# Optimization experiments

Hardware: AMD Instinct MI355X
Metric: run time of the kernel (lower is better)

## Reference

```python
import jax, jax.numpy as jnp
import numpy as np

B, S, D, H, HZ = 4096, 64, 9, 128, 32
DT = 0.1


def _lstm_cell(x, h, c, Wih, Whh, bih, bhh):
    gates = x @ Wih.T + bih + h @ Whh.T + bhh
    i, f, g, o = jnp.split(gates, 4, axis=-1)
    c_new = jax.nn.sigmoid(f) * c + jax.nn.sigmoid(i) * jnp.tanh(g)
    h_new = jax.nn.sigmoid(o) * jnp.tanh(c_new)
    return h_new, c_new


def _forward(input_batch, W_ih_enc, W_hh_enc, b_ih_enc, b_hh_enc, W_e, V_e, v_e,
             W_d, V_d, v_d, W_ih_dec, W_hh_dec, b_ih_dec, b_hh_dec,
             W_out, b_out, scaler_mean, scaler_std, pos_mean):
    bsz = input_batch.shape[0]
    # ---- encoder with input attention ----
    x_perm = jnp.swapaxes(input_batch, 1, 2)          # (B, D, S)
    attn_input = jnp.einsum('bds,ts->bdt', x_perm, V_e)  # V_e * x^i, precomputed once
    h0 = jnp.zeros((bsz, H), input_batch.dtype)
    c0 = jnp.zeros((bsz, H), input_batch.dtype)

    def enc_step(carry, x_t):
        h, c = carry
        attn_hidden = jnp.concatenate([h, c], axis=1) @ W_e.T          # (B, S)
        comb = jnp.tanh(attn_hidden[:, None, :] + attn_input)          # (B, D, S)
        e = comb @ v_e                                                 # (B, D)
        alpha = jax.nn.softmax(e, axis=1)
        h, c = _lstm_cell(alpha * x_t, h, c, W_ih_enc, W_hh_enc, b_ih_enc, b_hh_enc)
        return (h, c), h

    (h_enc, c_enc), hs = jax.lax.scan(enc_step, (h0, c0), jnp.swapaxes(input_batch, 0, 1))
    enc_hidden = jnp.swapaxes(hs, 0, 1)               # (B, S, H)
    attn_encoder = enc_hidden @ V_d.T                 # V_d * h_j, precomputed once

    # ---- initial physics state ----
    pos = input_batch[:, -1, :3] + pos_mean
    vel = input_batch[:, -1, 3:6] * scaler_std + scaler_mean
    pre_vel = input_batch[:, -2, 3:6] * scaler_std + scaler_mean
    acc = (vel - pre_vel) / DT

    def dec_step(carry, _):
        d, c, pos, vel, acc = carry
        attn_dec = jnp.concatenate([d, c], axis=1) @ W_d.T             # (B, H)
        comb = jnp.tanh(attn_dec[:, None, :] + attn_encoder)           # (B, S, H)
        beta = jax.nn.softmax(comb @ v_d, axis=1)                      # (B, S)
        context = jnp.einsum('bs,bsh->bh', beta, enc_hidden)           # (B, H)
        phys = jnp.concatenate([pos - pos_mean,
                                (vel - scaler_mean) / scaler_std,
                                acc / scaler_std], axis=1)             # (B, 9)
        d, c = _lstm_cell(jnp.concatenate([phys, context], axis=1), d, c,
                          W_ih_dec, W_hh_dec, b_ih_dec, b_hh_dec)
        pred_acc = (jnp.concatenate([d, context], axis=1) @ W_out.T + b_out) * scaler_std
        pos_pred = pos + vel * DT + 0.5 * acc * DT * DT                # Verlet position
        vel_new = vel + 0.5 * (acc + pred_acc) * DT                    # Verlet velocity
        out = jnp.concatenate([pos_pred, vel_new, pred_acc], axis=1)   # (B, 9)
        return (d, c, pos_pred, vel_new, pred_acc), out

    _, outs = jax.lax.scan(dec_step, (h_enc, c_enc, pos, vel, acc), None, length=HZ)
    return jnp.swapaxes(outs, 0, 1)                   # (B, HZ, 9)


def setup_inputs() -> dict:
    key = jax.random.key(0)
    ks = jax.random.split(key, 16)
    p = lambda k, shape, s=0.05: jax.random.normal(k, shape, dtype=jnp.float32) * s
    return dict(
        input_batch=jax.random.normal(ks[0], (B, S, D), dtype=jnp.float32),
        W_ih_enc=p(ks[1], (4 * H, D)), W_hh_enc=p(ks[2], (4 * H, H)),
        b_ih_enc=jnp.zeros((4 * H,), jnp.float32), b_hh_enc=jnp.zeros((4 * H,), jnp.float32),
        W_e=p(ks[3], (S, 2 * H)), V_e=p(ks[4], (S, S)), v_e=p(ks[5], (S,)),
        W_d=p(ks[6], (H, 2 * H)), V_d=p(ks[7], (H, H)), v_d=p(ks[8], (H,)),
        W_ih_dec=p(ks[9], (4 * H, 9 + H)), W_hh_dec=p(ks[10], (4 * H, H)),
        b_ih_dec=jnp.zeros((4 * H,), jnp.float32), b_hh_dec=jnp.zeros((4 * H,), jnp.float32),
        W_out=p(ks[11], (3, 2 * H)), b_out=jnp.zeros((3,), jnp.float32),
        scaler_mean=p(ks[12], (3,), 0.1),
        scaler_std=jnp.abs(p(ks[13], (3,), 0.1)) + 1.0,
        pos_mean=p(ks[14], (3,), 0.1),
    )


def reference(input_batch, W_ih_enc, W_hh_enc, b_ih_enc, b_hh_enc, W_e, V_e, v_e,
              W_d, V_d, v_d, W_ih_dec, W_hh_dec, b_ih_dec, b_hh_dec,
              W_out, b_out, scaler_mean, scaler_std, pos_mean):
    return _forward(input_batch, W_ih_enc, W_hh_enc, b_ih_enc, b_hh_enc, W_e, V_e, v_e,
                    W_d, V_d, v_d, W_ih_dec, W_hh_dec, b_ih_dec, b_hh_dec,
                    W_out, b_out, scaler_mean, scaler_std, pos_mean)
```

## Files before the change

### kernel.cpp

```cpp
#include <hip/hip_runtime.h>
#include <hip/hip_bf16.h>
#include <hip/hip_fp8.h>

#define B_   4096
#define S_   64
#define D_   9
#define H_   128
#define HZ_  32
#define DT_  0.1f

#define OFF_WET    0
#define OFF_VET    16384
#define OFF_WENCT  20480
#define OFF_BENC   90624
#define OFF_WDT    91136
#define OFF_WDECT  123904
#define OFF_BDEC   259584
#define OFF_WOUTT  260096
#define OFF_VDT    260864
#define OFF_DECD   277248
#define OFF_DECC   801536
#define F32_TOTAL  1325824
#define PREP_N     277248


typedef __bf16 bf16x8 __attribute__((ext_vector_type(8)));
typedef float  f32x4  __attribute__((ext_vector_type(4)));

__device__ __forceinline__ float fast_tanh(float x) {
    float e = __expf(2.0f * x);
    return 1.0f - __fdividef(2.0f, e + 1.0f);
}
__device__ __forceinline__ float sigf(float x) {
    return __fdividef(1.0f, 1.0f + __expf(-x));
}
__device__ __forceinline__ float bf_lo(unsigned int u) { return __uint_as_float(u << 16); }
__device__ __forceinline__ float bf_hi(unsigned int u) { return __uint_as_float(u & 0xffff0000u); }
__device__ __forceinline__ float bfu2f(unsigned short u) { return __uint_as_float((unsigned int)u << 16); }
__device__ __forceinline__ unsigned short f2bfu(float f) {
    __hip_bfloat16 b = __float2bfloat16(f);
    return *(unsigned short*)&b;
}
__device__ __forceinline__ unsigned int pack_bf(float lo, float hi) {
    return (unsigned int)f2bfu(lo) | ((unsigned int)f2bfu(hi) << 16);
}
__device__ __forceinline__ float f8tof(unsigned int byte) {
    __hip_fp8_e4m3 t; t.__x = (unsigned char)byte; return (float)t;
}
__device__ __forceinline__ unsigned char f2f8(float f) {
    __hip_fp8_e4m3 q(f); return q.__x;
}
__device__ __forceinline__ unsigned int pack4_f8(float a, float b, float c, float d) {
    return (unsigned int)f2f8(a) | ((unsigned int)f2f8(b) << 8) |
           ((unsigned int)f2f8(c) << 16) | ((unsigned int)f2f8(d) << 24);
}

__global__ void prep_kernel(const float* __restrict__ Wih_e, const float* __restrict__ Whh_e,
    const float* __restrict__ bih_e, const float* __restrict__ bhh_e,
    const float* __restrict__ W_e, const float* __restrict__ V_e,
    const float* __restrict__ W_d, const float* __restrict__ V_d,
    const float* __restrict__ Wih_d, const float* __restrict__ Whh_d,
    const float* __restrict__ bih_d, const float* __restrict__ bhh_d,
    const float* __restrict__ W_out, float* __restrict__ ws) {
  for (int idx = blockIdx.x * blockDim.x + threadIdx.x; idx < PREP_N;
       idx += gridDim.x * blockDim.x) {
    int i = idx;
    if (i < 16384) { continue; }
    i -= 16384;
    if (i < 4096) { int s = i >> 6, t = i & 63; ws[OFF_VET + i] = V_e[t * 64 + s]; continue; }
    i -= 4096;
    if (i < 70144) { continue; }
    i -= 70144;
    if (i < 512) { ws[OFF_BENC + i] = bih_e[i] + bhh_e[i]; continue; }
    i -= 512;
    if (i < 32768) { continue; }
    i -= 32768;
    if (i < 135680) { continue; }
    i -= 135680;
    if (i < 512) { ws[OFF_BDEC + i] = bih_d[i] + bhh_d[i]; continue; }
    i -= 512;
    if (i < 768) { int k = i / 3, j = i % 3; ws[OFF_WOUTT + i] = W_out[j * 256 + k]; continue; }
  }
}

__global__ void prep_mfma_kernel(const float* __restrict__ W_d,
    const float* __restrict__ Wih_d, const float* __restrict__ Whh_d,
    unsigned short* __restrict__ WdTm, unsigned short* __restrict__ WdecTm) {
  int idx = blockIdx.x * blockDim.x + threadIdx.x;
  if (idx < 32768) {
    int j = idx & 7, l = (idx >> 3) & 63, t = idx >> 9;
    int nt = t & 7, ks = t >> 3;
    int k = ks * 32 + (l >> 4) * 8 + j;
// ... 166 lines not shown
        g4[q] = acc;
      }
      #pragma unroll
      for (int r = 0; r < 4; ++r) {
        int m = quad * 4 + r;
        float gi = g4[0][r] + bbq[0];
        float gf = g4[1][r] + bbq[1];
        float gg = g4[2][r] + bbq[2];
        float go = g4[3][r] + bbq[3];
        float co = cF[m * 132 + ig];
        float cn = sigf(gf) * co + sigf(gi) * fast_tanh(gg);
        float hn = sigf(go) * fast_tanh(cn);
        cF[m * 132 + ig] = cn;
        bufN[m * 296 + ig] = f2bfu(hn);
        bufN[m * 296 + 128 + ig] = f2bfu(cn);
        EH[((size_t)(b0 + m) * S_ + t) * H_ + ig] = __float2bfloat16(hn);
      }
    }
    __syncthreads();
  }
  for (int i = tid; i < 16 * 128; i += 512) {
    int m = i >> 7, ii = i & 127;
    dG[(size_t)(b0 + m) * 128 + ii] = hA[0][m * 296 + ii];
    cG[(size_t)(b0 + m) * 128 + ii] = cF[m * 132 + ii];
  }
}

__global__ __launch_bounds__(256) void attnenc_mfma_kernel(
    const unsigned short* __restrict__ EH, const unsigned short* __restrict__ VdTm,
    unsigned char* __restrict__ AETf8, unsigned char* __restrict__ EHf8) {
  const int tid = threadIdx.x;
  const int b = blockIdx.x * 4 + (tid >> 6);
  const int l = tid & 63;
  const int quad = l >> 4, l15 = l & 15;

  const unsigned short* ehb = EH + (size_t)b * 8192;
  uint4 A[4][4];
  #pragma unroll
  for (int st = 0; st < 4; ++st)
    #pragma unroll
    for (int ks = 0; ks < 4; ++ks)
      A[st][ks] = *(const uint4*)(ehb + (st * 16 + l15) * 128 + ks * 32 + quad * 8);

  {
    unsigned char* e8b = EHf8 + (size_t)b * 8192;
    #pragma unroll
    for (int st = 0; st < 4; ++st)
      #pragma unroll
      for (int ks = 0; ks < 4; ++ks) {
        uint4 a = A[st][ks];
        uint2 pk;
        pk.x = pack4_f8(bf_lo(a.x), bf_hi(a.x), bf_lo(a.y), bf_hi(a.y));
        pk.y = pack4_f8(bf_lo(a.z), bf_hi(a.z), bf_lo(a.w), bf_hi(a.w));
        *(uint2*)(e8b + (st * 16 + l15) * 128 + ks * 32 + quad * 8) = pk;
      }
  }

  unsigned char* outb = AETf8 + (size_t)b * 8192;
  const int k = l15;
  #pragma unroll
  for (int nt = 0; nt < 8; ++nt) {
    uint4 Bf[4];
    #pragma unroll
    for (int ks = 0; ks < 4; ++ks)
      Bf[ks] = *(const uint4*)(VdTm + (size_t)((ks * 8 + nt) * 64 + l) * 8);
    int kg = nt * 16 + k;
    int kb = kg >> 3, k7 = kg & 7;
    #pragma unroll
    for (int st = 0; st < 4; ++st) {
      f32x4 acc = {0.f, 0.f, 0.f, 0.f};
      #pragma unroll
      for (int ks = 0; ks < 4; ++ks)
        acc = __builtin_amdgcn_mfma_f32_16x16x32_bf16(
            __builtin_bit_cast(bf16x8, A[st][ks]), __builtin_bit_cast(bf16x8, Bf[ks]), acc, 0, 0, 0);
      #pragma unroll
      for (int r = 0; r < 4; ++r) {
        int s = st * 16 + quad * 4 + r;
        outb[kb * 512 + s * 8 + k7] = f2f8(acc[r]);
      }
    }
  }
}

__global__ __launch_bounds__(256) void init_dec_kernel(
    const float* __restrict__ x_in,
    const unsigned short* __restrict__ dG, const float* __restrict__ cG,
    const unsigned short* __restrict__ WdTm,
    const float* __restrict__ smean_g, const float* __restrict__ sstd_g,
    const float* __restrict__ pmean_g,
    unsigned short* __restrict__ adG, float* __restrict__ pvsG) {
  __shared__ unsigned short dcB[16 * 264];
  const int tid = threadIdx.x;
  const int b0 = blockIdx.x * 16;
  const int l = tid & 63, w = tid >> 6;
  const int quad = l >> 4, l15 = l & 15;

  {
    int m = tid >> 4, i0 = (tid & 15) * 8;
    *(uint4*)&dcB[m * 264 + i0] = *(const uint4*)(dG + (size_t)(b0 + m) * 128 + i0);
    float4 c0 = *(const float4*)(cG + (size_t)(b0 + m) * 128 + i0);
    float4 c1 = *(const float4*)(cG + (size_t)(b0 + m) * 128 + i0 + 4);
    uint4 pk;
    pk.x = pack_bf(c0.x, c0.y); pk.y = pack_bf(c0.z, c0.w);
    pk.z = pack_bf(c1.x, c1.y); pk.w = pack_bf(c1.z, c1.w);
    *(uint4*)&dcB[m * 264 + 128 + i0] = pk;
  }
  if (tid < 48) {
    int m = tid / 3, jj = tid % 3;
    const float* xi = x_in + (size_t)(b0 + m) * 576;
    float sm = smean_g[jj], ss = sstd_g[jj], pm = pmean_g[jj];
    float v  = xi[63 * 9 + 3 + jj] * ss + sm;
    float pv = xi[62 * 9 + 3 + jj] * ss + sm;
    float* P = pvsG + (size_t)(b0 + m) * 12;
    P[jj] = xi[63 * 9 + jj] + pm;
    P[3 + jj] = v;
    P[6 + jj] = (v - pv) / DT_;
  }
  __syncthreads();
  #pragma unroll
  for (int t = 0; t < 2; ++t) {
    const int nt = w + 4 * t;
    f32x4 acc = {0.f, 0.f, 0.f, 0.f};
    #pragma unroll
    for (int ks = 0; ks < 8; ++ks) {
      uint4 au = *(const uint4*)&dcB[l15 * 264 + ks * 32 + quad * 8];
      uint4 bu = *(const uint4*)(WdTm + (size_t)((ks * 8 + nt) * 64 + l) * 8);
      acc = __builtin_amdgcn_mfma_f32_16x16x32_bf16(
          __builtin_bit_cast(bf16x8, au), __builtin_bit_cast(bf16x8, bu), acc, 0, 0, 0);
    }
    int n = nt * 16 + l15;
    #pragma unroll
    for (int r = 0; r < 4; ++r)
      adG[(size_t)(b0 + quad * 4 + r) * 128 + n] = f2bfu(acc[r]);
  }
}

__global__ __launch_bounds__(512, 2) void dec_step_kernel(
    const float* __restrict__ ws,
    const unsigned char* __restrict__ AETf8, const unsigned char* __restrict__ EHf8,
    const unsigned short* __restrict__ dG_in, float* __restrict__ cG,
    const unsigned short* __restrict__ WdTm, const unsigned short* __restrict__ WdecTm,
    unsigned short* __restrict__ dG_out, unsigned short* __restrict__ adG,
    float* __restrict__ pvsG, const float* __restrict__ v_d_g,
    const float* __restrict__ b_out_g, const float* __restrict__ smean_g,
    const float* __restrict__ sstd_g, const float* __restrict__ pmean_g,
    float* __restrict__ out, int hz) {
  __shared__ unsigned short adL[16 * 128];
  __shared__ float vdL[128];
  __shared__ float bet[16 * 64];
  __shared__ unsigned short gA[16 * 296];
  __shared__ unsigned short dcB[16 * 264];
  __shared__ float pd[16 * 3 * 8];
  __shared__ float pc[16 * 3 * 4];

  const int tid = threadIdx.x;
  const int b0 = blockIdx.x * 16;
  const int l = tid & 63, w = tid >> 6;
  const int quad = l >> 4, l15 = l & 15;

  if (tid < 256) {
    int m = tid >> 4, i0 = (tid & 15) * 8;
    *(uint4*)&gA[m * 296 + i0] = *(const uint4*)(dG_in + (size_t)(b0 + m) * 128 + i0);
  } else {
    int t = tid - 256;
    int m = t >> 4, i0 = (t & 15) * 8;
    *(uint4*)&adL[m * 128 + i0] = *(const uint4*)(adG + (size_t)(b0 + m) * 128 + i0);
  }
  if (tid < 128) vdL[tid] = v_d_g[tid];
  if (tid < 496) { int mm = tid / 31, r = tid % 31; gA[mm * 296 + 265 + r] = 0; }
  if (tid < 48) {
    int m = tid / 3, jj = tid % 3;
    const float* P = pvsG + (size_t)(b0 + m) * 12;
    float sm = smean_g[jj], ss = sstd_g[jj], pm = pmean_g[jj];
    gA[m * 296 + 256 + jj]     = f2bfu(P[jj] - pm);
    gA[m * 296 + 256 + 3 + jj] = f2bfu((P[3 + jj] - sm) / ss);
    gA[m * 296 + 256 + 6 + jj] = f2bfu(P[6 + jj] / ss);
  }
  __syncthreads();

  #pragma unroll
  for (int u = 0; u < 2; ++u) {
    const int mi = 2 * w + u;
    const unsigned char* aet = AETf8 + (size_t)(b0 + mi) * 8192;
    const unsigned short* adp = adL + mi * 128;
    float e = 0.f;
    #pragma unroll
    for (int kb = 0; kb < 16; ++kb) {
      uint2 av = *(const uint2*)(aet + kb * 512 + l * 8);
      uint4 ad8 = *(const uint4*)(adp + kb * 8);
      float4 v0 = *(const float4*)&vdL[kb * 8];
      float4 v1 = *(const float4*)&vdL[kb * 8 + 4];
      e += fast_tanh(bf_lo(ad8.x) + f8tof(av.x))       * v0.x;
      e += fast_tanh(bf_hi(ad8.x) + f8tof(av.x >> 8))  * v0.y;
      e += fast_tanh(bf_lo(ad8.y) + f8tof(av.x >> 16)) * v0.z;
      e += fast_tanh(bf_hi(ad8.y) + f8tof(av.x >> 24)) * v0.w;
      e += fast_tanh(bf_lo(ad8.z) + f8tof(av.y))       * v1.x;
      e += fast_tanh(bf_hi(ad8.z) + f8tof(av.y >> 8))  * v1.y;
      e += fast_tanh(bf_lo(ad8.w) + f8tof(av.y >> 16)) * v1.z;
      e += fast_tanh(bf_hi(ad8.w) + f8tof(av.y >> 24)) * v1.w;
    }
    float ex = __expf(e);
    float ss = ex;
    #pragma unroll
    for (int off = 32; off; off >>= 1) ss += __shfl_xor(ss, off, 64);
    bet[mi * 64 + l] = __fdividef(ex, ss);
  }
  #pragma unroll
  for (int u = 0; u < 2; ++u) {
    const int mi = 2 * w + u;
    const unsigned char* base = EHf8 + (size_t)(b0 + mi) * 8192;
    float a[8];
    #pragma unroll
    for (int r = 0; r < 8; ++r) a[r] = 0.f;
    #pragma unroll
    for (int it = 0; it < 16; ++it) {
      int sl = it * 4 + quad;
      uint2 ev = *(const uint2*)(base + sl * 128 + l15 * 8);
      float bt = bet[mi * 64 + sl];
      a[0] += bt * f8tof(ev.x);       a[1] += bt * f8tof(ev.x >> 8);
      a[2] += bt * f8tof(ev.x >> 16); a[3] += bt * f8tof(ev.x >> 24);
      a[4] += bt * f8tof(ev.y);       a[5] += bt * f8tof(ev.y >> 8);
      a[6] += bt * f8tof(ev.y >> 16); a[7] += bt * f8tof(ev.y >> 24);
    }
    #pragma unroll
    for (int r = 0; r < 8; ++r) {
      a[r] += __shfl_xor(a[r], 16, 64);
      a[r] += __shfl_xor(a[r], 32, 64);
    }
    if (quad == 0) {
      uint4 pk;
      pk.x = pack_bf(a[0], a[1]); pk.y = pack_bf(a[2], a[3]);
      pk.z = pack_bf(a[4], a[5]); pk.w = pack_bf(a[6], a[7]);
      *(uint4*)&gA[mi * 296 + 128 + l15 * 8] = pk;
    }
  }
  __syncthreads();

  {
    uint4 af[9];
    #pragma unroll
    for (int ks = 0; ks < 9; ++ks)
      af[ks] = *(const uint4*)&gA[l15 * 296 + ks * 32 + quad * 8];
    const int is = w, i = is * 16 + l15;
    float bb[4], wd[3];
    #pragma unroll
    for (int q = 0; q < 4; ++q) bb[q] = ws[OFF_BDEC + q * 128 + i];
    #pragma unroll
    for (int jj = 0; jj < 3; ++jj) wd[jj] = ws[OFF_WOUTT + i * 3 + jj];
    f32x4 g4[4];
    #pragma unroll
    for (int q = 0; q < 4; ++q) {
      f32x4 acc = {0.f, 0.f, 0.f, 0.f};
      #pragma unroll
      for (int ks = 0; ks < 9; ++ks) {
        uint4 bu = *(const uint4*)(WdecTm + (size_t)(((is * 4 + q) * 9 + ks) * 64 + l) * 8);
        acc = __builtin_amdgcn_mfma_f32_16x16x32_bf16(
            __builtin_bit_cast(bf16x8, af[ks]), __builtin_bit_cast(bf16x8, bu), acc, 0, 0, 0);
      }
      g4[q] = acc;
    }
    float pr[4][3];
    #pragma unroll
    for (int r = 0; r < 4; ++r) {
      int m = quad * 4 + r;
      float gi = g4[0][r] + bb[0];
      float gf = g4[1][r] + bb[1];
      float gg = g4[2][r] + bb[2];
      float go = g4[3][r] + bb[3];
      float co = cG[(size_t)(b0 + m) * 128 + i];
      float cn = sigf(gf) * co + sigf(gi) * fast_tanh(gg);
      float hn = sigf(go) * fast_tanh(cn);
      cG[(size_t)(b0 + m) * 128 + i] = cn;
      unsigned short hb = f2bfu(hn);
      dG_out[(size_t)(b0 + m) * 128 + i] = hb;
      dcB[m * 264 + i] = hb;
      dcB[m * 264 + 128 + i] = f2bfu(cn);
      pr[r][0] = hn * wd[0]; pr[r][1] = hn * wd[1]; pr[r][2] = hn * wd[2];
    }
    #pragma unroll
    for (int r = 0; r < 4; ++r)
      #pragma unroll
      for (int jj = 0; jj < 3; ++jj) {
        float v = pr[r][jj];
        #pragma unroll
        for (int off = 8; off; off >>= 1) v += __shfl_xor(v, off, 64);
        pr[r][jj] = v;
      }
    if (l15 == 0) {
      #pragma unroll
      for (int r = 0; r < 4; ++r)
        #pragma unroll
        for (int jj = 0; jj < 3; ++jj)
          pd[((quad * 4 + r) * 3 + jj) * 8 + is] = pr[r][jj];
    }
  }
  __syncthreads();

  {
    const int nt = w;
    f32x4 acc = {0.f, 0.f, 0.f, 0.f};
    #pragma unroll
    for (int ks = 0; ks < 8; ++ks) {
      uint4 au = *(const uint4*)&dcB[l15 * 264 + ks * 32 + quad * 8];
      uint4 bu = *(const uint4*)(WdTm + (size_t)((ks * 8 + nt) * 64 + l) * 8);
      acc = __builtin_amdgcn_mfma_f32_16x16x32_bf16(
          __builtin_bit_cast(bf16x8, au), __builtin_bit_cast(bf16x8, bu), acc, 0, 0, 0);
    }
    int n = nt * 16 + l15;
    #pragma unroll
    for (int r = 0; r < 4; ++r) {
      int m = quad * 4 + r;
      adG[(size_t)(b0 + m) * 128 + n] = f2bfu(acc[r]);
    }
  }
  if (tid < 192) {
    int m = tid / 12, jj = (tid % 12) / 4, part = tid % 4;
    int k0 = part * 32;
    float acc = 0.f;
    for (int k = k0; k < k0 + 32; ++k) {
      __hip_bfloat16 hv = *(__hip_bfloat16*)&gA[m * 296 + 128 + k];
      acc += __bfloat162float(hv) * ws[OFF_WOUTT + 384 + k * 3 + jj];
    }
    pc[(m * 3 + jj) * 4 + part] = acc;
  }
  __syncthreads();

  if (tid < 48) {
    int m = tid / 3, jj = tid % 3;
    float s = b_out_g[jj];
    #pragma unroll
    for (int p = 0; p < 4; ++p) s += pc[(m * 3 + jj) * 4 + p];
    #pragma unroll
    for (int is = 0; is < 8; ++is) s += pd[(m * 3 + jj) * 8 + is];
    float pacc = s * sstd_g[jj];
    float* P = pvsG + (size_t)(b0 + m) * 12;
    float pos = P[jj], vel = P[3 + jj], acc = P[6 + jj];
    float ppred = pos + vel * DT_ + 0.5f * acc * DT_ * DT_;
    float vnew  = vel + 0.5f * (acc + pacc) * DT_;
    size_t ob = ((size_t)(b0 + m) * HZ_ + hz) * 9;
    out[ob + jj] = ppred; out[ob + 3 + jj] = vnew; out[ob + 6 + jj] = pacc;
    P[jj] = ppred; P[3 + jj] = vnew; P[6 + jj] = pacc;
  }
}

extern "C" void kernel_launch(void* const* d_in, const int* in_sizes, int n_in,
                              void* d_out, int out_size, void* d_ws, size_t ws_size,
                              hipStream_t stream) {
  (void)in_sizes; (void)n_in; (void)out_size; (void)ws_size;
  const float* x      = (const float*)d_in[0];
  const float* Wih_e  = (const float*)d_in[1];
  const float* Whh_e  = (const float*)d_in[2];
  const float* bih_e  = (const float*)d_in[3];
  const float* bhh_e  = (const float*)d_in[4];
  const float* W_e    = (const float*)d_in[5];
  const float* V_e    = (const float*)d_in[6];
  const float* v_e    = (const float*)d_in[7];
  const float* W_d    = (const float*)d_in[8];
  const float* V_d    = (const float*)d_in[9];
  const float* v_d    = (const float*)d_in[10];
  const float* Wih_d  = (const float*)d_in[11];
  const float* Whh_d  = (const float*)d_in[12];
  const float* bih_d  = (const float*)d_in[13];
  const float* bhh_d  = (const float*)d_in[14];
  const float* W_out  = (const float*)d_in[15];
  const float* b_out  = (const float*)d_in[16];
  const float* smean  = (const float*)d_in[17];
  const float* sstd   = (const float*)d_in[18];
  const float* pmean  = (const float*)d_in[19];

  float* ws = (float*)d_ws;
  float* pvsG = ws;
  unsigned short* WeTm   = (unsigned short*)(ws + OFF_WET);
  unsigned short* WencTm = (unsigned short*)(ws + OFF_WENCT);
  unsigned short* WdTm   = (unsigned short*)(ws + OFF_WDT);
  unsigned short* WdecTm = (unsigned short*)(ws + OFF_WDECT);
  unsigned short* VdTm   = (unsigned short*)(ws + OFF_VDT);
  unsigned short* dG     = (unsigned short*)(ws + OFF_DECD);
  float* cG = ws + OFF_DECC;
  unsigned short* ub  = (unsigned short*)(ws + F32_TOTAL);
  unsigned short* EH  = ub;
  unsigned char*  AETf8 = (unsigned char*)(ub + 33554432);
  unsigned char*  EHf8  = AETf8 + (size_t)B_ * 8192;
  unsigned short* adG = ub + 67108864;
  float* out = (float*)d_out;

  prep_kernel<<<(PREP_N + 255) / 256, 256, 0, stream>>>(
      Wih_e, Whh_e, bih_e, bhh_e, W_e, V_e, W_d, V_d,
      Wih_d, Whh_d, bih_d, bhh_d, W_out, ws);
  prep_mfma_kernel<<<(32768 + 147456 + 255) / 256, 256, 0, stream>>>(
      W_d, Wih_d, Whh_d, WdTm, WdecTm);
  prep_enc_mfma_kernel<<<(16384 + 81920 + 16384 + 255) / 256, 256, 0, stream>>>(
      W_e, Wih_e, Whh_e, V_d, WeTm, WencTm, VdTm);
  encoder_mfma_kernel<<<B_ / 16, 512, 0, stream>>>(
      x, ws, v_e, WeTm, WencTm, (__hip_bfloat16*)EH, dG, cG);
  attnenc_mfma_kernel<<<B_ / 4, 256, 0, stream>>>(EH, VdTm, AETf8, EHf8);
  init_dec_kernel<<<B_ / 16, 256, 0, stream>>>(
      x, dG, cG, WdTm, smean, sstd, pmean, adG, pvsG);
  for (int hz = 0; hz < HZ_; ++hz) {
    dec_step_kernel<<<B_ / 16, 512, 0, stream>>>(
        ws, AETf8, EHf8, dG, cG, WdTm, WdecTm, dG, adG, pvsG,
        v_d, b_out, smean, sstd, pmean, out, hz);
  }
}
```

Baseline: 1.938 ms.

## Split decoder step into separate attention and GEMM kernels for higher occupancy

The per-step decoder kernel is split in two. A lightweight attention kernel uses one wave per batch row across 1024 small blocks to compute attention scores, softmax and context, and writes the context to a global bf16 buffer. A GEMM kernel then loads that context into shared memory and runs the LSTM and output MFMA work. The aim is more parallelism and latency hiding for the memory-heavy fp8 attention reads, at the cost of an extra launch per step and a global round trip for the context.

```diff
diff --git a/kernel.cpp b/kernel.cpp
--- a/kernel.cpp
+++ b/kernel.cpp
@@ -393,19 +393,84 @@
   }
 }
 
-__global__ __launch_bounds__(512, 2) void dec_step_kernel(
+__global__ __launch_bounds__(256, 8) void attn_step_kernel(
+    const unsigned char* __restrict__ AETf8, const unsigned char* __restrict__ EHf8,
+    const unsigned short* __restrict__ adG, const float* __restrict__ v_d_g,
+    unsigned short* __restrict__ ctxG) {
+  __shared__ unsigned short adL[4][128];
+  __shared__ float vdL[128];
+
+  const int tid = threadIdx.x;
+  const int l = tid & 63, w = tid >> 6;
+  const int b = blockIdx.x * 4 + w;
+  const int quad = l >> 4, l15 = l & 15;
+
+  if (l < 16)
+    *(uint4*)&adL[w][l * 8] = *(const uint4*)(adG + (size_t)b * 128 + l * 8);
+  if (tid < 32)
+    *(float4*)&vdL[tid * 4] = *(const float4*)(v_d_g + tid * 4);
+  __syncthreads();
+
+  const unsigned char* aet = AETf8 + (size_t)b * 8192;
+  float e = 0.f;
+  #pragma unroll
+  for (int kb = 0; kb < 16; ++kb) {
+    uint2 av = *(const uint2*)(aet + kb * 512 + l * 8);
+    uint4 ad8 = *(const uint4*)&adL[w][kb * 8];
+    float4 v0 = *(const float4*)&vdL[kb * 8];
+    float4 v1 = *(const float4*)&vdL[kb * 8 + 4];
+    e += fast_tanh(bf_lo(ad8.x) + f8tof(av.x))       * v0.x;
+    e += fast_tanh(bf_hi(ad8.x) + f8tof(av.x >> 8))  * v0.y;
+    e += fast_tanh(bf_lo(ad8.y) + f8tof(av.x >> 16)) * v0.z;
+    e += fast_tanh(bf_hi(ad8.y) + f8tof(av.x >> 24)) * v0.w;
+    e += fast_tanh(bf_lo(ad8.z) + f8tof(av.y))       * v1.x;
+    e += fast_tanh(bf_hi(ad8.z) + f8tof(av.y >> 8))  * v1.y;
+    e += fast_tanh(bf_lo(ad8.w) + f8tof(av.y >> 16)) * v1.z;
+    e += fast_tanh(bf_hi(ad8.w) + f8tof(av.y >> 24)) * v1.w;
+  }
+  float ex = __expf(e);
+  float ss = ex;
+  #pragma unroll
+  for (int off = 32; off; off >>= 1) ss += __shfl_xor(ss, off, 64);
+  const float bet = __fdividef(ex, ss);
+
+  const unsigned char* base = EHf8 + (size_t)b * 8192;
+  float a[8];
+  #pragma unroll
+  for (int r = 0; r < 8; ++r) a[r] = 0.f;
+  #pragma unroll
+  for (int it = 0; it < 16; ++it) {
+    int sl = it * 4 + quad;
+    uint2 ev = *(const uint2*)(base + sl * 128 + l15 * 8);
+    float bt = __shfl(bet, sl, 64);
+    a[0] += bt * f8tof(ev.x);       a[1] += bt * f8tof(ev.x >> 8);
+    a[2] += bt * f8tof(ev.x >> 16); a[3] += bt * f8tof(ev.x >> 24);
+    a[4] += bt * f8tof(ev.y);       a[5] += bt * f8tof(ev.y >> 8);
+    a[6] += bt * f8tof(ev.y >> 16); a[7] += bt * f8tof(ev.y >> 24);
+  }
+  #pragma unroll
+  for (int r = 0; r < 8; ++r) {
+    a[r] += __shfl_xor(a[r], 16, 64);
+    a[r] += __shfl_xor(a[r], 32, 64);
+  }
+  if (quad == 0) {
+    uint4 pk;
+    pk.x = pack_bf(a[0], a[1]); pk.y = pack_bf(a[2], a[3]);
+    pk.z = pack_bf(a[4], a[5]); pk.w = pack_bf(a[6], a[7]);
+    *(uint4*)(ctxG + (size_t)b * 128 + l15 * 8) = pk;
+  }
+}
+
+__global__ __launch_bounds__(512, 2) void gemm_step_kernel(
     const float* __restrict__ ws,
-    const unsigned char* __restrict__ AETf8, const unsigned char* __restrict__ EHf8,
     const unsigned short* __restrict__ dG_in, float* __restrict__ cG,
+    const unsigned short* __restrict__ ctxG,
     const unsigned short* __restrict__ WdTm, const unsigned short* __restrict__ WdecTm,
     unsigned short* __restrict__ dG_out, unsigned short* __restrict__ adG,
-    float* __restrict__ pvsG, const float* __restrict__ v_d_g,
+    float* __restrict__ pvsG,
     const float* __restrict__ b_out_g, const float* __restrict__ smean_g,
     const float* __restrict__ sstd_g, const float* __restrict__ pmean_g,
     float* __restrict__ out, int hz) {
-  __shared__ unsigned short adL[16 * 128];
-  __shared__ float vdL[128];
-  __shared__ float bet[16 * 64];
   __shared__ unsigned short gA[16 * 296];
   __shared__ unsigned short dcB[16 * 264];
   __shared__ float pd[16 * 3 * 8];
@@ -422,9 +487,8 @@
   } else {
     int t = tid - 256;
     int m = t >> 4, i0 = (t & 15) * 8;
-    *(uint4*)&adL[m * 128 + i0] = *(const uint4*)(adG + (size_t)(b0 + m) * 128 + i0);
-  }
-  if (tid < 128) vdL[tid] = v_d_g[tid];
+    *(uint4*)&gA[m * 296 + 128 + i0] = *(const uint4*)(ctxG + (size_t)(b0 + m) * 128 + i0);
+  }
   if (tid < 496) { int mm = tid / 31, r = tid % 31; gA[mm * 296 + 265 + r] = 0; }
   if (tid < 48) {
     int m = tid / 3, jj = tid % 3;
@@ -433,64 +497,6 @@
     gA[m * 296 + 256 + jj]     = f2bfu(P[jj] - pm);
     gA[m * 296 + 256 + 3 + jj] = f2bfu((P[3 + jj] - sm) / ss);
     gA[m * 296 + 256 + 6 + jj] = f2bfu(P[6 + jj] / ss);
-  }
-  __syncthreads();
-
-  #pragma unroll
-  for (int u = 0; u < 2; ++u) {
-    const int mi = 2 * w + u;
-    const unsigned char* aet = AETf8 + (size_t)(b0 + mi) * 8192;
-    const unsigned short* adp = adL + mi * 128;
-    float e = 0.f;
-    #pragma unroll
-    for (int kb = 0; kb < 16; ++kb) {
-      uint2 av = *(const uint2*)(aet + kb * 512 + l * 8);
-      uint4 ad8 = *(const uint4*)(adp + kb * 8);
-      float4 v0 = *(const float4*)&vdL[kb * 8];
-      float4 v1 = *(const float4*)&vdL[kb * 8 + 4];
-      e += fast_tanh(bf_lo(ad8.x) + f8tof(av.x))       * v0.x;
-      e += fast_tanh(bf_hi(ad8.x) + f8tof(av.x >> 8))  * v0.y;
-      e += fast_tanh(bf_lo(ad8.y) + f8tof(av.x >> 16)) * v0.z;
-      e += fast_tanh(bf_hi(ad8.y) + f8tof(av.x >> 24)) * v0.w;
-      e += fast_tanh(bf_lo(ad8.z) + f8tof(av.y))       * v1.x;
-      e += fast_tanh(bf_hi(ad8.z) + f8tof(av.y >> 8))  * v1.y;
-      e += fast_tanh(bf_lo(ad8.w) + f8tof(av.y >> 16)) * v1.z;
-      e += fast_tanh(bf_hi(ad8.w) + f8tof(av.y >> 24)) * v1.w;
-    }
-    float ex = __expf(e);
-    float ss = ex;
-    #pragma unroll
-    for (int off = 32; off; off >>= 1) ss += __shfl_xor(ss, off, 64);
-    bet[mi * 64 + l] = __fdividef(ex, ss);
-  }
-  #pragma unroll
-  for (int u = 0; u < 2; ++u) {
-    const int mi = 2 * w + u;
-    const unsigned char* base = EHf8 + (size_t)(b0 + mi) * 8192;
-    float a[8];
-    #pragma unroll
-    for (int r = 0; r < 8; ++r) a[r] = 0.f;
-    #pragma unroll
-    for (int it = 0; it < 16; ++it) {
-      int sl = it * 4 + quad;
-      uint2 ev = *(const uint2*)(base + sl * 128 + l15 * 8);
-      float bt = bet[mi * 64 + sl];
-      a[0] += bt * f8tof(ev.x);       a[1] += bt * f8tof(ev.x >> 8);
-      a[2] += bt * f8tof(ev.x >> 16); a[3] += bt * f8tof(ev.x >> 24);
-      a[4] += bt * f8tof(ev.y);       a[5] += bt * f8tof(ev.y >> 8);
-      a[6] += bt * f8tof(ev.y >> 16); a[7] += bt * f8tof(ev.y >> 24);
-    }
-    #pragma unroll
-    for (int r = 0; r < 8; ++r) {
-      a[r] += __shfl_xor(a[r], 16, 64);
-      a[r] += __shfl_xor(a[r], 32, 64);
-    }
-    if (quad == 0) {
-      uint4 pk;
-      pk.x = pack_bf(a[0], a[1]); pk.y = pack_bf(a[2], a[3]);
-      pk.z = pack_bf(a[4], a[5]); pk.w = pack_bf(a[6], a[7]);
-      *(uint4*)&gA[mi * 296 + 128 + l15 * 8] = pk;
-    }
   }
   __syncthreads();
 
@@ -634,6 +640,7 @@
   unsigned short* WdecTm = (unsigned short*)(ws + OFF_WDECT);
   unsigned short* VdTm   = (unsigned short*)(ws + OFF_VDT);
   unsigned short* dG     = (unsigned short*)(ws + OFF_DECD);
+  unsigned short* ctxG   = dG + 524288;
   float* cG = ws + OFF_DECC;
   unsigned short* ub  = (unsigned short*)(ws + F32_TOTAL);
   unsigned short* EH  = ub;
@@ -655,8 +662,9 @@
   init_dec_kernel<<<B_ / 16, 256, 0, stream>>>(
       x, dG, cG, WdTm, smean, sstd, pmean, adG, pvsG);
   for (int hz = 0; hz < HZ_; ++hz) {
-    dec_step_kernel<<<B_ / 16, 512, 0, stream>>>(
-        ws, AETf8, EHf8, dG, cG, WdTm, WdecTm, dG, adG, pvsG,
-        v_d, b_out, smean, sstd, pmean, out, hz);
-  }
-}
+    attn_step_kernel<<<B_ / 4, 256, 0, stream>>>(AETf8, EHf8, adG, v_d, ctxG);
+    gemm_step_kernel<<<B_ / 16, 512, 0, stream>>>(
+        ws, dG, cG, ctxG, WdTm, WdecTm, dG, adG, pvsG,
+        b_out, smean, sstd, pmean, out, hz);
+  }
+}
```

After: 1.702 ms. -12.2%, faster.

## Fuse decoder init and all horizon steps into one persistent per-batch kernel

Applied to the files above, without the earlier changes.

Replaces the decoder init kernel and the 32 per-step decoder launches with a single kernel. Each block owns 4 batch rows and loops over the horizon. Per-row attention-encoder and encoder-hidden fp8 tiles are staged once into LDS, and LSTM state, hidden and physics state stay in registers or LDS instead of going through global memory every step. This removes repeated launches and repeated global reloads of the large per-row tiles. The cost is that MFMA tiles now carry only 4 valid rows out of 16, so much of the matrix work is wasted, and LDS use per block is large.

```diff
diff --git a/kernel.cpp b/kernel.cpp
--- a/kernel.cpp
+++ b/kernel.cpp
@@ -8,6 +8,7 @@
 #define H_   128
 #define HZ_  32
 #define DT_  0.1f
+#define PB   4
 
 #define OFF_WET    0
 #define OFF_VET    16384
@@ -340,264 +341,269 @@
   }
 }
 
-__global__ __launch_bounds__(256) void init_dec_kernel(
-    const float* __restrict__ x_in,
+__global__ __launch_bounds__(256, 2) void dec_persist_kernel(
+    const float* __restrict__ ws,
+    const unsigned char* __restrict__ AETf8, const unsigned char* __restrict__ EHf8,
     const unsigned short* __restrict__ dG, const float* __restrict__ cG,
-    const unsigned short* __restrict__ WdTm,
-    const float* __restrict__ smean_g, const float* __restrict__ sstd_g,
-    const float* __restrict__ pmean_g,
-    unsigned short* __restrict__ adG, float* __restrict__ pvsG) {
-  __shared__ unsigned short dcB[16 * 264];
+    const unsigned short* __restrict__ WdTm, const unsigned short* __restrict__ WdecTm,
+    const float* __restrict__ x_in, const float* __restrict__ v_d_g,
+    const float* __restrict__ b_out_g, const float* __restrict__ smean_g,
+    const float* __restrict__ sstd_g, const float* __restrict__ pmean_g,
+    float* __restrict__ out) {
+  __shared__ unsigned char aetL[PB][8192];
+  __shared__ unsigned char ehL[PB][8192];
+  __shared__ unsigned short adL[PB][128];
+  __shared__ unsigned short gA[PB][296];
+  __shared__ unsigned short dcB[PB][264];
+  __shared__ float vdL[128];
+  __shared__ float pvs[PB][12];
+  __shared__ float pd[PB * 3 * 8];
+  __shared__ float pc[PB * 3 * 4];
+
   const int tid = threadIdx.x;
-  const int b0 = blockIdx.x * 16;
+  const int b0 = blockIdx.x * PB;
   const int l = tid & 63, w = tid >> 6;
   const int quad = l >> 4, l15 = l & 15;
+  const int arow = l15 & 3;
 
   {
-    int m = tid >> 4, i0 = (tid & 15) * 8;
-    *(uint4*)&dcB[m * 264 + i0] = *(const uint4*)(dG + (size_t)(b0 + m) * 128 + i0);
-    float4 c0 = *(const float4*)(cG + (size_t)(b0 + m) * 128 + i0);
-    float4 c1 = *(const float4*)(cG + (size_t)(b0 + m) * 128 + i0 + 4);
-    uint4 pk;
-    pk.x = pack_bf(c0.x, c0.y); pk.y = pack_bf(c0.z, c0.w);
-    pk.z = pack_bf(c1.x, c1.y); pk.w = pack_bf(c1.z, c1.w);
-    *(uint4*)&dcB[m * 264 + 128 + i0] = pk;
-  }
-  if (tid < 48) {
+    const uint4* ga = (const uint4*)(AETf8 + (size_t)b0 * 8192);
+    const uint4* ge = (const uint4*)(EHf8 + (size_t)b0 * 8192);
+    uint4* la = (uint4*)aetL;
+    uint4* le = (uint4*)ehL;
+    for (int i = tid; i < PB * 512; i += 256) { la[i] = ga[i]; le[i] = ge[i]; }
+  }
+  for (int i = tid; i < PB * 128; i += 256) {
+    int m = i >> 7, ii = i & 127;
+    unsigned short dv = dG[(size_t)(b0 + m) * 128 + ii];
+    gA[m][ii] = dv;
+    dcB[m][ii] = dv;
+    dcB[m][128 + ii] = f2bfu(cG[(size_t)(b0 + m) * 128 + ii]);
+  }
+  if (tid < PB * 31) { int mm = tid / 31, r = tid % 31; gA[mm][265 + r] = 0; }
+  if (tid < 128) vdL[tid] = v_d_g[tid];
+  if (tid < PB * 3) {
     int m = tid / 3, jj = tid % 3;
     const float* xi = x_in + (size_t)(b0 + m) * 576;
     float sm = smean_g[jj], ss = sstd_g[jj], pm = pmean_g[jj];
     float v  = xi[63 * 9 + 3 + jj] * ss + sm;
     float pv = xi[62 * 9 + 3 + jj] * ss + sm;
-    float* P = pvsG + (size_t)(b0 + m) * 12;
-    P[jj] = xi[63 * 9 + jj] + pm;
-    P[3 + jj] = v;
-    P[6 + jj] = (v - pv) / DT_;
-  }
-  __syncthreads();
+    pvs[m][jj] = xi[63 * 9 + jj] + pm;
+    pvs[m][3 + jj] = v;
+    pvs[m][6 + jj] = (v - pv) / DT_;
+  }
+  float bbq[2][4], wdq[2][3];
   #pragma unroll
   for (int t = 0; t < 2; ++t) {
-    const int nt = w + 4 * t;
+    int i = (2 * w + t) * 16 + l15;
+    #pragma unroll
+    for (int q = 0; q < 4; ++q) bbq[t][q] = ws[OFF_BDEC + q * 128 + i];
+    #pragma unroll
+    for (int jj = 0; jj < 3; ++jj) wdq[t][jj] = ws[OFF_WOUTT + i * 3 + jj];
+  }
+  float creg[2][4];
+  if (quad == 0) {
+    #pragma unroll
+    for (int t = 0; t < 2; ++t) {
+      int i = (2 * w + t) * 16 + l15;
+      #pragma unroll
+      for (int m = 0; m < PB; ++m) creg[t][m] = cG[(size_t)(b0 + m) * 128 + i];
+    }
+  }
+  __syncthreads();
+
+  #pragma unroll
+  for (int t = 0; t < 2; ++t) {
+    const int nt = 2 * w + t;
     f32x4 acc = {0.f, 0.f, 0.f, 0.f};
     #pragma unroll
     for (int ks = 0; ks < 8; ++ks) {
-      uint4 au = *(const uint4*)&dcB[l15 * 264 + ks * 32 + quad * 8];
+      uint4 au = *(const uint4*)&dcB[arow][ks * 32 + quad * 8];
       uint4 bu = *(const uint4*)(WdTm + (size_t)((ks * 8 + nt) * 64 + l) * 8);
       acc = __builtin_amdgcn_mfma_f32_16x16x32_bf16(
           __builtin_bit_cast(bf16x8, au), __builtin_bit_cast(bf16x8, bu), acc, 0, 0, 0);
     }
-    int n = nt * 16 + l15;
-    #pragma unroll
-    for (int r = 0; r < 4; ++r)
-      adG[(size_t)(b0 + quad * 4 + r) * 128 + n] = f2bfu(acc[r]);
-  }
-}
-
-__global__ __launch_bounds__(512, 2) void dec_step_kernel(
-    const float* __restrict__ ws,
-    const unsigned char* __restrict__ AETf8, const unsigned char* __restrict__ EHf8,
-    const unsigned short* __restrict__ dG_in, float* __restrict__ cG,
-    const unsigned short* __restrict__ WdTm, const unsigned short* __restrict__ WdecTm,
-    unsigned short* __restrict__ dG_out, unsigned short* __restrict__ adG,
-    float* __restrict__ pvsG, const float* __restrict__ v_d_g,
-    const float* __restrict__ b_out_g, const float* __restrict__ smean_g,
-    const float* __restrict__ sstd_g, const float* __restrict__ pmean_g,
-    float* __restrict__ out, int hz) {
-  __shared__ unsigned short adL[16 * 128];
-  __shared__ float vdL[128];
-  __shared__ float bet[16 * 64];
-  __shared__ unsigned short gA[16 * 296];
-  __shared__ unsigned short dcB[16 * 264];
-  __shared__ float pd[16 * 3 * 8];
-  __shared__ float pc[16 * 3 * 4];
-
-  const int tid = threadIdx.x;
-  const int b0 = blockIdx.x * 16;
-  const int l = tid & 63, w = tid >> 6;
-  const int quad = l >> 4, l15 = l & 15;
-
-  if (tid < 256) {
-    int m = tid >> 4, i0 = (tid & 15) * 8;
-    *(uint4*)&gA[m * 296 + i0] = *(const uint4*)(dG_in + (size_t)(b0 + m) * 128 + i0);
-  } else {
-    int t = tid - 256;
-    int m = t >> 4, i0 = (t & 15) * 8;
-    *(uint4*)&adL[m * 128 + i0] = *(const uint4*)(adG + (size_t)(b0 + m) * 128 + i0);
-  }
-  if (tid < 128) vdL[tid] = v_d_g[tid];
-  if (tid < 496) { int mm = tid / 31, r = tid % 31; gA[mm * 296 + 265 + r] = 0; }
-  if (tid < 48) {
-    int m = tid / 3, jj = tid % 3;
-    const float* P = pvsG + (size_t)(b0 + m) * 12;
-    float sm = smean_g[jj], ss = sstd_g[jj], pm = pmean_g[jj];
-    gA[m * 296 + 256 + jj]     = f2bfu(P[jj] - pm);
-    gA[m * 296 + 256 + 3 + jj] = f2bfu((P[3 + jj] - sm) / ss);
-    gA[m * 296 + 256 + 6 + jj] = f2bfu(P[6 + jj] / ss);
+    if (quad == 0) {
+      #pragma unroll
+      for (int r = 0; r < 4; ++r)
+        adL[r][nt * 16 + l15] = f2bfu(acc[r]);
+    }
   }
   __syncthreads();
 
-  #pragma unroll
-  for (int u = 0; u < 2; ++u) {
-    const int mi = 2 * w + u;
-    const unsigned char* aet = AETf8 + (size_t)(b0 + mi) * 8192;
-    const unsigned short* adp = adL + mi * 128;
-    float e = 0.f;
-    #pragma unroll
-    for (int kb = 0; kb < 16; ++kb) {
-      uint2 av = *(const uint2*)(aet + kb * 512 + l * 8);
-      uint4 ad8 = *(const uint4*)(adp + kb * 8);
-      float4 v0 = *(const float4*)&vdL[kb * 8];
-      float4 v1 = *(const float4*)&vdL[kb * 8 + 4];
-      e += fast_tanh(bf_lo(ad8.x) + f8tof(av.x))       * v0.x;
-      e += fast_tanh(bf_hi(ad8.x) + f8tof(av.x >> 8))  * v0.y;
-      e += fast_tanh(bf_lo(ad8.y) + f8tof(av.x >> 16)) * v0.z;
-      e += fast_tanh(bf_hi(ad8.y) + f8tof(av.x >> 24)) * v0.w;
-      e += fast_tanh(bf_lo(ad8.z) + f8tof(av.y))       * v1.x;
-      e += fast_tanh(bf_hi(ad8.z) + f8tof(av.y >> 8))  * v1.y;
-      e += fast_tanh(bf_lo(ad8.w) + f8tof(av.y >> 16)) * v1.z;
-      e += fast_tanh(bf_hi(ad8.w) + f8tof(av.y >> 24)) * v1.w;
-    }
-    float ex = __expf(e);
-    float ss = ex;
-    #pragma unroll
-    for (int off = 32; off; off >>= 1) ss += __shfl_xor(ss, off, 64);
-    bet[mi * 64 + l] = __fdividef(ex, ss);
-  }
-  #pragma unroll
-  for (int u = 0; u < 2; ++u) {
-    const int mi = 2 * w + u;
-    const unsigned char* base = EHf8 + (size_t)(b0 + mi) * 8192;
-    float a[8];
-    #pragma unroll
-    for (int r = 0; r < 8; ++r) a[r] = 0.f;
-    #pragma unroll
-    for (int it = 0; it < 16; ++it) {
-      int sl = it * 4 + quad;
-      uint2 ev = *(const uint2*)(base + sl * 128 + l15 * 8);
-      float bt = bet[mi * 64 + sl];
-      a[0] += bt * f8tof(ev.x);       a[1] += bt * f8tof(ev.x >> 8);
-      a[2] += bt * f8tof(ev.x >> 16); a[3] += bt * f8tof(ev.x >> 24);
-      a[4] += bt * f8tof(ev.y);       a[5] += bt * f8tof(ev.y >> 8);
-      a[6] += bt * f8tof(ev.y >> 16); a[7] += bt * f8tof(ev.y >> 24);
-    }
-    #pragma unroll
-    for (int r = 0; r < 8; ++r) {
-      a[r] += __shfl_xor(a[r], 16, 64);
-      a[r] += __shfl_xor(a[r], 32, 64);
+  for (int hz = 0; hz < HZ_; ++hz) {
+    float bet;
+    {
+      const unsigned char* aet = aetL[w];
+      float e = 0.f;
+      #pragma unroll
+      for (int kb = 0; kb < 16; ++kb) {
+        uint2 av = *(const uint2*)(aet + kb * 512 + l * 8);
+        uint4 ad8 = *(const uint4*)&adL[w][kb * 8];
+        float4 v0 = *(const float4*)&vdL[kb * 8];
+        float4 v1 = *(const float4*)&vdL[kb * 8 + 4];
+        e += fast_tanh(bf_lo(ad8.x) + f8tof(av.x))       * v0.x;
+        e += fast_tanh(bf_hi(ad8.x) + f8tof(av.x >> 8))  * v0.y;
+        e += fast_tanh(bf_lo(ad8.y) + f8tof(av.x >> 16)) * v0.z;
+        e += fast_tanh(bf_hi(ad8.y) + f8tof(av.x >> 24)) * v0.w;
+        e += fast_tanh(bf_lo(ad8.z) + f8tof(av.y))       * v1.x;
+        e += fast_tanh(bf_hi(ad8.z) + f8tof(av.y >> 8))  * v1.y;
+        e += fast_tanh(bf_lo(ad8.w) + f8tof(av.y >> 16)) * v1.z;
+        e += fast_tanh(bf_hi(ad8.w) + f8tof(av.y >> 24)) * v1.w;
+      }
+      float ex = __expf(e);
+      float ss = ex;
+      #pragma unroll
+      for (int off = 32; off; off >>= 1) ss += __shfl_xor(ss, off, 64);
+      bet = __fdividef(ex, ss);
+    }
+    {
+      const unsigned char* base = ehL[w];
+      float a[8];
+      #pragma unroll
+      for (int r = 0; r < 8; ++r) a[r] = 0.f;
+      #pragma unroll
+      for (int it = 0; it < 16; ++it) {
+        int sl = it * 4 + quad;
+        uint2 ev = *(const uint2*)(base + sl * 128 + l15 * 8);
+        float bt = __shfl(bet, sl, 64);
+        a[0] += bt * f8tof(ev.x);       a[1] += bt * f8tof(ev.x >> 8);
+        a[2] += bt * f8tof(ev.x >> 16); a[3] += bt * f8tof(ev.x >> 24);
+        a[4] += bt * f8tof(ev.y);       a[5] += bt * f8tof(ev.y >> 8);
+        a[6] += bt * f8tof(ev.y >> 16); a[7] += bt * f8tof(ev.y >> 24);
+      }
+      #pragma unroll
+      for (int r = 0; r < 8; ++r) {
+        a[r] += __shfl_xor(a[r], 16, 64);
+        a[r] += __shfl_xor(a[r], 32, 64);
+      }
+      if (quad == 0) {
+        uint4 pk;
+        pk.x = pack_bf(a[0], a[1]); pk.y = pack_bf(a[2], a[3]);
+        pk.z = pack_bf(a[4], a[5]); pk.w = pack_bf(a[6], a[7]);
+        *(uint4*)&gA[w][128 + l15 * 8] = pk;
+      }
+    }
+    if (tid < PB * 3) {
+      int m = tid / 3, jj = tid % 3;
+      float sm = smean_g[jj], ss = sstd_g[jj], pm = pmean_g[jj];
+      gA[m][256 + jj]     = f2bfu(pvs[m][jj] - pm);
+      gA[m][256 + 3 + jj] = f2bfu((pvs[m][3 + jj] - sm) / ss);
+      gA[m][256 + 6 + jj] = f2bfu(pvs[m][6 + jj] / ss);
+    }
+    __syncthreads();
+
+    unsigned short hbr[2][4];
+    {
+      uint4 af[9];
+      #pragma unroll
+      for (int ks = 0; ks < 9; ++ks)
+        af[ks] = *(const uint4*)&gA[arow][ks * 32 + quad * 8];
+      #pragma unroll
+      for (int t = 0; t < 2; ++t) {
+        const int is = 2 * w + t;
+        const int i = is * 16 + l15;
+        f32x4 g4[4];
+        #pragma unroll
+        for (int q = 0; q < 4; ++q) {
+          f32x4 acc = {0.f, 0.f, 0.f, 0.f};
+          #pragma unroll
+          for (int ks = 0; ks < 9; ++ks) {
+            uint4 bu = *(const uint4*)(WdecTm + (size_t)(((is * 4 + q) * 9 + ks) * 64 + l) * 8);
+            acc = __builtin_amdgcn_mfma_f32_16x16x32_bf16(
+                __builtin_bit_cast(bf16x8, af[ks]), __builtin_bit_cast(bf16x8, bu), acc, 0, 0, 0);
+          }
+          g4[q] = acc;
+        }
+        if (quad == 0) {
+          float pr[4][3];
+          #pragma unroll
+          for (int r = 0; r < 4; ++r) {
+            float gi = g4[0][r] + bbq[t][0];
+            float gf = g4[1][r] + bbq[t][1];
+            float gg = g4[2][r] + bbq[t][2];
+            float go = g4[3][r] + bbq[t][3];
+            float co = creg[t][r];
+            float cn = sigf(gf) * co + sigf(gi) * fast_tanh(gg);
+            float hn = sigf(go) * fast_tanh(cn);
+            creg[t][r] = cn;
+            unsigned short hb = f2bfu(hn);
+            dcB[r][i] = hb;
+            dcB[r][128 + i] = f2bfu(cn);
+            hbr[t][r] = hb;
+            pr[r][0] = hn * wdq[t][0]; pr[r][1] = hn * wdq[t][1]; pr[r][2] = hn * wdq[t][2];
+          }
+          #pragma unroll
+          for (int r = 0; r < 4; ++r)
+            #pragma unroll
+            for (int jj = 0; jj < 3; ++jj) {
+              float v = pr[r][jj];
+              #pragma unroll
+              for (int off = 8; off; off >>= 1) v += __shfl_xor(v, off, 64);
+              pr[r][jj] = v;
+            }
+          if (l15 == 0) {
+            #pragma unroll
+            for (int r = 0; r < 4; ++r)
+              #pragma unroll
+              for (int jj = 0; jj < 3; ++jj)
+                pd[(r * 3 + jj) * 8 + is] = pr[r][jj];
+          }
+        }
+      }
+    }
+    __syncthreads();
+
+    #pragma unroll
+    for (int t = 0; t < 2; ++t) {
+      const int nt = 2 * w + t;
+      f32x4 acc = {0.f, 0.f, 0.f, 0.f};
+      #pragma unroll
+      for (int ks = 0; ks < 8; ++ks) {
+        uint4 au = *(const uint4*)&dcB[arow][ks * 32 + quad * 8];
+        uint4 bu = *(const uint4*)(WdTm + (size_t)((ks * 8 + nt) * 64 + l) * 8);
+        acc = __builtin_amdgcn_mfma_f32_16x16x32_bf16(
+            __builtin_bit_cast(bf16x8, au), __builtin_bit_cast(bf16x8, bu), acc, 0, 0, 0);
+      }
+      if (quad == 0) {
+        #pragma unroll
+        for (int r = 0; r < 4; ++r)
+          adL[r][nt * 16 + l15] = f2bfu(acc[r]);
+      }
     }
     if (quad == 0) {
-      uint4 pk;
-      pk.x = pack_bf(a[0], a[1]); pk.y = pack_bf(a[2], a[3]);
-      pk.z = pack_bf(a[4], a[5]); pk.w = pack_bf(a[6], a[7]);
-      *(uint4*)&gA[mi * 296 + 128 + l15 * 8] = pk;
-    }
-  }
-  __syncthreads();
-
-  {
-    uint4 af[9];
-    #pragma unroll
-    for (int ks = 0; ks < 9; ++ks)
-      af[ks] = *(const uint4*)&gA[l15 * 296 + ks * 32 + quad * 8];
-    const int is = w, i = is * 16 + l15;
-    float bb[4], wd[3];
-    #pragma unroll
-    for (int q = 0; q < 4; ++q) bb[q] = ws[OFF_BDEC + q * 128 + i];
-    #pragma unroll
-    for (int jj = 0; jj < 3; ++jj) wd[jj] = ws[OFF_WOUTT + i * 3 + jj];
-    f32x4 g4[4];
-    #pragma unroll
-    for (int q = 0; q < 4; ++q) {
-      f32x4 acc = {0.f, 0.f, 0.f, 0.f};
-      #pragma unroll
-      for (int ks = 0; ks < 9; ++ks) {
-        uint4 bu = *(const uint4*)(WdecTm + (size_t)(((is * 4 + q) * 9 + ks) * 64 + l) * 8);
-        acc = __builtin_amdgcn_mfma_f32_16x16x32_bf16(
-            __builtin_bit_cast(bf16x8, af[ks]), __builtin_bit_cast(bf16x8, bu), acc, 0, 0, 0);
-      }
-      g4[q] = acc;
-    }
-    float pr[4][3];
-    #pragma unroll
-    for (int r = 0; r < 4; ++r) {
-      int m = quad * 4 + r;
-      float gi = g4[0][r] + bb[0];
-      float gf = g4[1][r] + bb[1];
-      float gg = g4[2][r] + bb[2];
-      float go = g4[3][r] + bb[3];
-      float co = cG[(size_t)(b0 + m) * 128 + i];
-      float cn = sigf(gf) * co + sigf(gi) * fast_tanh(gg);
-      float hn = sigf(go) * fast_tanh(cn);
-      cG[(size_t)(b0 + m) * 128 + i] = cn;
-      unsigned short hb = f2bfu(hn);
-      dG_out[(size_t)(b0 + m) * 128 + i] = hb;
-      dcB[m * 264 + i] = hb;
-      dcB[m * 264 + 128 + i] = f2bfu(cn);
-      pr[r][0] = hn * wd[0]; pr[r][1] = hn * wd[1]; pr[r][2] = hn * wd[2];
-    }
-    #pragma unroll
-    for (int r = 0; r < 4; ++r)
-      #pragma unroll
-      for (int jj = 0; jj < 3; ++jj) {
-        float v = pr[r][jj];
+      #pragma unroll
+      for (int t = 0; t < 2; ++t) {
+        int i = (2 * w + t) * 16 + l15;
         #pragma unroll
-        for (int off = 8; off; off >>= 1) v += __shfl_xor(v, off, 64);
-        pr[r][jj] = v;
-      }
-    if (l15 == 0) {
-      #pragma unroll
-      for (int r = 0; r < 4; ++r)
-        #pragma unroll
-        for (int jj = 0; jj < 3; ++jj)
-          pd[((quad * 4 + r) * 3 + jj) * 8 + is] = pr[r][jj];
-    }
-  }
-  __syncthreads();
-
-  {
-    const int nt = w;
-    f32x4 acc = {0.f, 0.f, 0.f, 0.f};
-    #pragma unroll
-    for (int ks = 0; ks < 8; ++ks) {
-      uint4 au = *(const uint4*)&dcB[l15 * 264 + ks * 32 + quad * 8];
-      uint4 bu = *(const uint4*)(WdTm + (size_t)((ks * 8 + nt) * 64 + l) * 8);
-      acc = __builtin_amdgcn_mfma_f32_16x16x32_bf16(
-          __builtin_bit_cast(bf16x8, au), __builtin_bit_cast(bf16x8, bu), acc, 0, 0, 0);
-    }
-    int n = nt * 16 + l15;
-    #pragma unroll
-    for (int r = 0; r < 4; ++r) {
-      int m = quad * 4 + r;
-      adG[(size_t)(b0 + m) * 128 + n] = f2bfu(acc[r]);
-    }
-  }
-  if (tid < 192) {
-    int m = tid / 12, jj = (tid % 12) / 4, part = tid % 4;
-    int k0 = part * 32;
-    float acc = 0.f;
-    for (int k = k0; k < k0 + 32; ++k) {
-      __hip_bfloat16 hv = *(__hip_bfloat16*)&gA[m * 296 + 128 + k];
-      acc += __bfloat162float(hv) * ws[OFF_WOUTT + 384 + k * 3 + jj];
-    }
-    pc[(m * 3 + jj) * 4 + part] = acc;
-  }
-  __syncthreads();
-
-  if (tid < 48) {
-    int m = tid / 3, jj = tid % 3;
-    float s = b_out_g[jj];
-    #pragma unroll
-    for (int p = 0; p < 4; ++p) s += pc[(m * 3 + jj) * 4 + p];
-    #pragma unroll
-    for (int is = 0; is < 8; ++is) s += pd[(m * 3 + jj) * 8 + is];
-    float pacc = s * sstd_g[jj];
-    float* P = pvsG + (size_t)(b0 + m) * 12;
-    float pos = P[jj], vel = P[3 + jj], acc = P[6 + jj];
-    float ppred = pos + vel * DT_ + 0.5f * acc * DT_ * DT_;
-    float vnew  = vel + 0.5f * (acc + pacc) * DT_;
-    size_t ob = ((size_t)(b0 + m) * HZ_ + hz) * 9;
-    out[ob + jj] = ppred; out[ob + 3 + jj] = vnew; out[ob + 6 + jj] = pacc;
-    P[jj] = ppred; P[3 + jj] = vnew; P[6 + jj] = pacc;
+        for (int r = 0; r < 4; ++r) gA[r][i] = hbr[t][r];
+      }
+    }
+    if (tid < PB * 12) {
+      int m = tid / 12, jj = (tid % 12) / 4, part = tid % 4;
+      int k0 = part * 32;
+      float acc = 0.f;
+      for (int k = k0; k < k0 + 32; ++k)
+        acc += bfu2f(gA[m][128 + k]) * ws[OFF_WOUTT + 384 + k * 3 + jj];
+      pc[(m * 3 + jj) * 4 + part] = acc;
+    }
+    __syncthreads();
+
+    if (tid < PB * 3) {
+      int m = tid / 3, jj = tid % 3;
+      float s = b_out_g[jj];
+      #pragma unroll
+      for (int p = 0; p < 4; ++p) s += pc[(m * 3 + jj) * 4 + p];
+      #pragma unroll
+      for (int is = 0; is < 8; ++is) s += pd[(m * 3 + jj) * 8 + is];
+      float pacc = s * sstd_g[jj];
+      float pos = pvs[m][jj], vel = pvs[m][3 + jj], acc = pvs[m][6 + jj];
+      float ppred = pos + vel * DT_ + 0.5f * acc * DT_ * DT_;
+      float vnew  = vel + 0.5f * (acc + pacc) * DT_;
+      size_t ob = ((size_t)(b0 + m) * HZ_ + hz) * 9;
+      out[ob + jj] = ppred; out[ob + 3 + jj] = vnew; out[ob + 6 + jj] = pacc;
+      pvs[m][jj] = ppred; pvs[m][3 + jj] = vnew; pvs[m][6 + jj] = pacc;
+    }
   }
 }
 
@@ -627,7 +633,6 @@
   const float* pmean  = (const float*)d_in[19];
 
   float* ws = (float*)d_ws;
-  float* pvsG = ws;
   unsigned short* WeTm   = (unsigned short*)(ws + OFF_WET);
   unsigned short* WencTm = (unsigned short*)(ws + OFF_WENCT);
   unsigned short* WdTm   = (unsigned short*)(ws + OFF_WDT);
@@ -639,7 +644,6 @@
   unsigned short* EH  = ub;
   unsigned char*  AETf8 = (unsigned char*)(ub + 33554432);
   unsigned char*  EHf8  = AETf8 + (size_t)B_ * 8192;
-  unsigned short* adG = ub + 67108864;
   float* out = (float*)d_out;
 
   prep_kernel<<<(PREP_N + 255) / 256, 256, 0, stream>>>(
@@ -652,11 +656,7 @@
   encoder_mfma_kernel<<<B_ / 16, 512, 0, stream>>>(
       x, ws, v_e, WeTm, WencTm, (__hip_bfloat16*)EH, dG, cG);
   attnenc_mfma_kernel<<<B_ / 4, 256, 0, stream>>>(EH, VdTm, AETf8, EHf8);
-  init_dec_kernel<<<B_ / 16, 256, 0, stream>>>(
-      x, dG, cG, WdTm, smean, sstd, pmean, adG, pvsG);
-  for (int hz = 0; hz < HZ_; ++hz) {
-    dec_step_kernel<<<B_ / 16, 512, 0, stream>>>(
-        ws, AETf8, EHf8, dG, cG, WdTm, WdecTm, dG, adG, pvsG,
-        v_d, b_out, smean, sstd, pmean, out, hz);
-  }
-}
+  dec_persist_kernel<<<B_ / PB, 256, 0, stream>>>(
+      ws, AETf8, EHf8, dG, cG, WdTm, WdecTm,
+      x, v_d, b_out, smean, sstd, pmean, out);
+}
```

New measurement: 3.801 ms. +96.1%, slower.
